# Kernel optimization log

Hardware: AMD Instinct MI355X
Metric: run time of the kernel (lower is better)

The kernel has to match this reference:

```python
import jax, jax.numpy as jnp
import numpy as np

N_NODES = 20000
N_EDGES = 640000
IN_DIM = 128
HID = 128
OUT_DIM = 3
N_GRAPHS = 32


def setup_inputs() -> dict:
    key = jax.random.key(0)
    ks = jax.random.split(key, 12)
    x = jax.random.normal(ks[0], (N_NODES, IN_DIM), dtype=jnp.float32)
    edge_index = jax.random.randint(ks[1], (2, N_EDGES), 0, N_NODES, dtype=jnp.int64)
    batch = jnp.sort(jax.random.randint(ks[2], (N_NODES,), 0, N_GRAPHS, dtype=jnp.int64))
    batch = batch.at[0].set(0).at[-1].set(N_GRAPHS - 1)
    s = 0.05
    W_gcn = jax.random.normal(ks[3], (IN_DIM, HID), jnp.float32) * s
    b_gcn = jnp.zeros((HID,), jnp.float32)
    W_sage_l = jax.random.normal(ks[4], (HID, HID), jnp.float32) * s  # neighbor branch
    W_sage_r = jax.random.normal(ks[5], (HID, HID), jnp.float32) * s  # root branch
    b_sage = jnp.zeros((HID,), jnp.float32)
    W_fc1 = jax.random.normal(ks[6], (HID, HID), jnp.float32) * s
    b_fc1 = jnp.zeros((HID,), jnp.float32)
    W_fc2 = jax.random.normal(ks[7], (HID, OUT_DIM), jnp.float32) * s
    b_fc2 = jnp.zeros((OUT_DIM,), jnp.float32)
    return {
        'x': x, 'edge_index': edge_index, 'batch': batch,
        'W_gcn': W_gcn, 'b_gcn': b_gcn,
        'W_sage_l': W_sage_l, 'W_sage_r': W_sage_r, 'b_sage': b_sage,
        'W_fc1': W_fc1, 'b_fc1': b_fc1, 'W_fc2': W_fc2, 'b_fc2': b_fc2,
    }


def reference(x, edge_index, batch, W_gcn, b_gcn, W_sage_l, W_sage_r, b_sage,
              W_fc1, b_fc1, W_fc2, b_fc2):
    n = x.shape[0]
    row, col = edge_index[0], edge_index[1]  # source -> target

    # ---- GCNConv: symmetric-normalized aggregation with self-loops ----
    h = x @ W_gcn  # [N, H]
    loops = jnp.arange(n, dtype=row.dtype)
    row_sl = jnp.concatenate([row, loops])
    col_sl = jnp.concatenate([col, loops])
    deg = jax.ops.segment_sum(jnp.ones_like(col_sl, dtype=h.dtype), col_sl,
                              num_segments=n)
    dinv = jnp.where(deg > 0, jax.lax.rsqrt(deg), 0.0)
    norm = dinv[row_sl] * dinv[col_sl]  # [E+N]
    h_gcn = jax.ops.segment_sum(h[row_sl] * norm[:, None], col_sl,
                                num_segments=n) + b_gcn
    h_gcn = jax.nn.relu(h_gcn)

    # ---- SAGEConv (mean aggregator) ----
    cnt = jax.ops.segment_sum(jnp.ones_like(col, dtype=h_gcn.dtype), col,
                              num_segments=n)
    neigh = jax.ops.segment_sum(h_gcn[row], col, num_segments=n)
    neigh = neigh / jnp.maximum(cnt, 1.0)[:, None]
    h_sage = neigh @ W_sage_l + h_gcn @ W_sage_r + b_sage
    h_sage = jax.nn.relu(h_sage)

    # ---- global_add_pool (num_graphs = 32 < 50) ----
    pooled = jax.ops.segment_sum(h_sage, batch, num_segments=N_GRAPHS)  # [G, H]

    # ---- MLP head ----
    out = jax.nn.relu(pooled @ W_fc1 + b_fc1) @ W_fc2 + b_fc2  # [G, 3]
    return out
```

## Files before the change

### kernel.cpp

```cpp
#include <hip/hip_runtime.h>

#define N_NODES 20000
#define N_EDGES 640000
#define HID 128
#define N_GRAPHS 32

#define SCAN_BLK 256
#define SCAN_NBLK ((N_NODES + SCAN_BLK - 1) / SCAN_BLK)

__global__ __launch_bounds__(256) void hist_k(const int* __restrict__ col,
                                              int* __restrict__ cnt) {
    int e = blockIdx.x * blockDim.x + threadIdx.x;
    if (e < N_EDGES) {
        int c = col[e];
        if ((unsigned)c < N_NODES) atomicAdd(&cnt[c], 1);
    }
}

__global__ __launch_bounds__(SCAN_BLK) void scanA_k(const int* __restrict__ cnt,
                                                    int* __restrict__ blkSum) {
    __shared__ int wsum[SCAN_BLK / 64];
    const int b = blockIdx.x, t = threadIdx.x;
    const int i = b * SCAN_BLK + t;
    int v = (i < N_NODES) ? cnt[i] : 0;
#pragma unroll
    for (int o = 1; o < 64; o <<= 1) v += __shfl_xor(v, o);
    if ((t & 63) == 0) wsum[t >> 6] = v;
    __syncthreads();
    if (t == 0) {
        int s = 0;
#pragma unroll
        for (int w = 0; w < SCAN_BLK / 64; ++w) s += wsum[w];
        blkSum[b] = s;
    }
}

__global__ __launch_bounds__(SCAN_BLK) void scanB_k(const int* __restrict__ cnt,
                                                    const int* __restrict__ blkSum,
                                                    int* __restrict__ offs,
                                                    int* __restrict__ cursor,
                                                    float* __restrict__ dinv) {
    __shared__ int sm[SCAN_BLK];
    __shared__ int base_s;
    const int b = blockIdx.x, t = threadIdx.x;
    const int i = b * SCAN_BLK + t;
    const int v = (i < N_NODES) ? cnt[i] : 0;
    sm[t] = v;
    if (t == 0) {
        int s = 0;
        for (int k = 0; k < b; ++k) s += blkSum[k];
        base_s = s;
    }
    __syncthreads();
    for (int o = 1; o < SCAN_BLK; o <<= 1) {
        int add = (t >= o) ? sm[t - o] : 0;
        __syncthreads();
        sm[t] += add;
        __syncthreads();
    }
    if (i < N_NODES) {
        int excl = base_s + ((t > 0) ? sm[t - 1] : 0);
        offs[i] = excl;
        cursor[i] = excl;
        dinv[i] = rsqrtf((float)(v + 1));
        if (i == N_NODES - 1) offs[N_NODES] = excl + v;
    }
}

__global__ __launch_bounds__(256) void fill_k(const int* __restrict__ row,
                                              const int* __restrict__ col,
                                              int* __restrict__ cursor,
                                              int* __restrict__ csr_src) {
    int e = blockIdx.x * blockDim.x + threadIdx.x;
    if (e < N_EDGES) {
        int c = col[e];
        int r = row[e];
        if ((unsigned)c < N_NODES && (unsigned)r < N_NODES) {
            int p = atomicAdd(&cursor[c], 1);
            csr_src[p] = r;
        }
    }
}

__global__ __launch_bounds__(256) void gemm128_k(const float* __restrict__ X,
                                                 const float* __restrict__ W,
                                                 float* __restrict__ Y,
                                                 int nrows) {
    __shared__ float ws[128 * 128];
    __shared__ float xs[32 * 128];
    const int t = threadIdx.x;
    for (int i = t; i < 4096; i += 256)
        ((float4*)ws)[i] = ((const float4*)W)[i];
    const int rg = t >> 5;
    const int c4 = (t & 31) * 4;
    const int ntiles = (nrows + 31) / 32;
    for (int tile = blockIdx.x; tile < ntiles; tile += gridDim.x) {
        const int row0 = tile * 32;
        __syncthreads();
#pragma unroll
        for (int i = 0; i < 4; ++i) {
            int idx = t + i * 256;
            int rr = row0 + (idx >> 5);
            float4 v = (rr < nrows) ? ((const float4*)X)[(size_t)rr * 32 + (idx & 31)]
                                    : make_float4(0.f, 0.f, 0.f, 0.f);
            ((float4*)xs)[idx] = v;
        }
        __syncthreads();
        float4 acc[4];
        acc[0] = acc[1] = acc[2] = acc[3] = make_float4(0.f, 0.f, 0.f, 0.f);
#pragma unroll 4
        for (int k = 0; k < 128; k += 2) {
            float4 w0 = *(const float4*)&ws[(k + 0) * 128 + c4];
            float4 w1 = *(const float4*)&ws[(k + 1) * 128 + c4];
#pragma unroll
            for (int i = 0; i < 4; ++i) {
                float2 xv = *(const float2*)&xs[(rg * 4 + i) * 128 + k];
                acc[i].x = fmaf(xv.x, w0.x, fmaf(xv.y, w1.x, acc[i].x));
                acc[i].y = fmaf(xv.x, w0.y, fmaf(xv.y, w1.y, acc[i].y));
                acc[i].z = fmaf(xv.x, w0.z, fmaf(xv.y, w1.z, acc[i].z));
                acc[i].w = fmaf(xv.x, w0.w, fmaf(xv.y, w1.w, acc[i].w));
            }
        }
#pragma unroll
        for (int i = 0; i < 4; ++i) {
            int rr = row0 + rg * 4 + i;
            if (rr < nrows) *(float4*)&Y[(size_t)rr * 128 + c4] = acc[i];
        }
    }
}

__global__ __launch_bounds__(256) void gcn_agg_k(const float* __restrict__ h,
                                                 const int* __restrict__ offs,
                                                 const int* __restrict__ src,
                                                 const float* __restrict__ dinv,
                                                 const float* __restrict__ bias,
                                                 float* __restrict__ out) {
    const int wave = threadIdx.x >> 6;
    const int lane = threadIdx.x & 63;
    const int half = lane >> 5;
    const int node = (blockIdx.x * 4 + wave) * 2 + half;
    const int c4 = (lane & 31) * 4;
    const int nd = (node < N_NODES) ? node : (N_NODES - 1);
    const float dc = dinv[nd];
    float4 hv = *(const float4*)&h[(size_t)nd * 128 + c4];
    float4 acc = make_float4(dc * hv.x, dc * hv.y, dc * hv.z, dc * hv.w);
    const int beg = offs[nd];
    const int deg = offs[nd + 1] - beg;
    const int mdeg = max(deg, __shfl(deg, lane ^ 32));
    for (int j = 0; j < mdeg; j += 4) {
        int i0 = (j + 0 < deg) ? beg + j + 0 : 0;
        int i1 = (j + 1 < deg) ? beg + j + 1 : 0;
        int i2 = (j + 2 < deg) ? beg + j + 2 : 0;
        int i3 = (j + 3 < deg) ? beg + j + 3 : 0;
        int s0 = src[i0], s1 = src[i1], s2 = src[i2], s3 = src[i3];
        float w0 = (j + 0 < deg) ? dinv[s0] : 0.f;
        float w1 = (j + 1 < deg) ? dinv[s1] : 0.f;
        float w2 = (j + 2 < deg) ? dinv[s2] : 0.f;
        float w3 = (j + 3 < deg) ? dinv[s3] : 0.f;
        float4 v0 = *(const float4*)&h[(size_t)s0 * 128 + c4];
        float4 v1 = *(const float4*)&h[(size_t)s1 * 128 + c4];
        float4 v2 = *(const float4*)&h[(size_t)s2 * 128 + c4];
        float4 v3 = *(const float4*)&h[(size_t)s3 * 128 + c4];
        acc.x = fmaf(w0, v0.x, fmaf(w1, v1.x, fmaf(w2, v2.x, fmaf(w3, v3.x, acc.x))));
        acc.y = fmaf(w0, v0.y, fmaf(w1, v1.y, fmaf(w2, v2.y, fmaf(w3, v3.y, acc.y))));
        acc.z = fmaf(w0, v0.z, fmaf(w1, v1.z, fmaf(w2, v2.z, fmaf(w3, v3.z, acc.z))));
        acc.w = fmaf(w0, v0.w, fmaf(w1, v1.w, fmaf(w2, v2.w, fmaf(w3, v3.w, acc.w))));
    }
    float4 b = *(const float4*)&bias[c4];
    float4 o;
    o.x = fmaxf(fmaf(dc, acc.x, b.x), 0.f);
    o.y = fmaxf(fmaf(dc, acc.y, b.y), 0.f);
    o.z = fmaxf(fmaf(dc, acc.z, b.z), 0.f);
    o.w = fmaxf(fmaf(dc, acc.w, b.w), 0.f);
    if (node < N_NODES) *(float4*)&out[(size_t)node * 128 + c4] = o;
}

__global__ __launch_bounds__(256) void sage_agg_k(const float* __restrict__ hg,
                                                  const int* __restrict__ offs,
                                                  const int* __restrict__ src,
                                                  float* __restrict__ out) {
    const int wave = threadIdx.x >> 6;
    const int lane = threadIdx.x & 63;
    const int half = lane >> 5;
    const int node = (blockIdx.x * 4 + wave) * 2 + half;
    const int c4 = (lane & 31) * 4;
    const int nd = (node < N_NODES) ? node : (N_NODES - 1);
    float4 acc = make_float4(0.f, 0.f, 0.f, 0.f);
    const int beg = offs[nd];
    const int deg = offs[nd + 1] - beg;
    const int mdeg = max(deg, __shfl(deg, lane ^ 32));
    for (int j = 0; j < mdeg; j += 4) {
        int i0 = (j + 0 < deg) ? beg + j + 0 : 0;
        int i1 = (j + 1 < deg) ? beg + j + 1 : 0;
        int i2 = (j + 2 < deg) ? beg + j + 2 : 0;
        int i3 = (j + 3 < deg) ? beg + j + 3 : 0;
        float w0 = (j + 0 < deg) ? 1.f : 0.f;
        float w1 = (j + 1 < deg) ? 1.f : 0.f;
        float w2 = (j + 2 < deg) ? 1.f : 0.f;
        float w3 = (j + 3 < deg) ? 1.f : 0.f;
        int s0 = src[i0], s1 = src[i1], s2 = src[i2], s3 = src[i3];
        float4 v0 = *(const float4*)&hg[(size_t)s0 * 128 + c4];
        float4 v1 = *(const float4*)&hg[(size_t)s1 * 128 + c4];
        float4 v2 = *(const float4*)&hg[(size_t)s2 * 128 + c4];
        float4 v3 = *(const float4*)&hg[(size_t)s3 * 128 + c4];
        acc.x = fmaf(w0, v0.x, fmaf(w1, v1.x, fmaf(w2, v2.x, fmaf(w3, v3.x, acc.x))));
        acc.y = fmaf(w0, v0.y, fmaf(w1, v1.y, fmaf(w2, v2.y, fmaf(w3, v3.y, acc.y))));
        acc.z = fmaf(w0, v0.z, fmaf(w1, v1.z, fmaf(w2, v2.z, fmaf(w3, v3.z, acc.z))));
        acc.w = fmaf(w0, v0.w, fmaf(w1, v1.w, fmaf(w2, v2.w, fmaf(w3, v3.w, acc.w))));
    }
    float inv = 1.0f / (float)max(deg, 1);
    float4 o;
    o.x = acc.x * inv;
    o.y = acc.y * inv;
    o.z = acc.z * inv;
    o.w = acc.w * inv;
    if (node < N_NODES) *(float4*)&out[(size_t)node * 128 + c4] = o;
}

__global__ __launch_bounds__(256) void combine_k(const float* __restrict__ An,
                                                 const float* __restrict__ Bh,
                                                 const float* __restrict__ Wl,
                                                 const float* __restrict__ Wr,
                                                 const float* __restrict__ bias,
                                                 float* __restrict__ Y) {
    __shared__ float ws[128 * 128];
    __shared__ float xs[32 * 128];
    const int t = threadIdx.x;
    const int rg = t >> 5;
    const int c4 = (t & 31) * 4;
    const int ntiles = (N_NODES + 31) / 32;
    for (int tile = blockIdx.x; tile < ntiles; tile += gridDim.x) {
        const int row0 = tile * 32;
        float4 acc[4];
        {
            float4 b = *(const float4*)&bias[c4];
            acc[0] = acc[1] = acc[2] = acc[3] = b;
        }
#pragma unroll
        for (int m = 0; m < 2; ++m) {
            const float* Wm = m ? Wr : Wl;
            const float* Xm = m ? Bh : An;
            __syncthreads();
            for (int i = t; i < 4096; i += 256)
                ((float4*)ws)[i] = ((const float4*)Wm)[i];
#pragma unroll
            for (int i = 0; i < 4; ++i) {
                int idx = t + i * 256;
                int rr = row0 + (idx >> 5);
                float4 v = (rr < N_NODES) ? ((const float4*)Xm)[(size_t)rr * 32 + (idx & 31)]
                                          : make_float4(0.f, 0.f, 0.f, 0.f);
                ((float4*)xs)[idx] = v;
            }
            __syncthreads();
#pragma unroll 4
            for (int k = 0; k < 128; k += 2) {
                float4 w0 = *(const float4*)&ws[(k + 0) * 128 + c4];
                float4 w1 = *(const float4*)&ws[(k + 1) * 128 + c4];
#pragma unroll
                for (int i = 0; i < 4; ++i) {
                    float2 xv = *(const float2*)&xs[(rg * 4 + i) * 128 + k];
                    acc[i].x = fmaf(xv.x, w0.x, fmaf(xv.y, w1.x, acc[i].x));
                    acc[i].y = fmaf(xv.x, w0.y, fmaf(xv.y, w1.y, acc[i].y));
                    acc[i].z = fmaf(xv.x, w0.z, fmaf(xv.y, w1.z, acc[i].z));
                    acc[i].w = fmaf(xv.x, w0.w, fmaf(xv.y, w1.w, acc[i].w));
                }
            }
        }
#pragma unroll
        for (int i = 0; i < 4; ++i) {
            int rr = row0 + rg * 4 + i;
            if (rr < N_NODES) {
                float4 o = acc[i];
                o.x = fmaxf(o.x, 0.f);
                o.y = fmaxf(o.y, 0.f);
                o.z = fmaxf(o.z, 0.f);
                o.w = fmaxf(o.w, 0.f);
                *(float4*)&Y[(size_t)rr * 128 + c4] = o;
            }
        }
    }
}

#define POOL_ROWS 64
__global__ __launch_bounds__(256) void pool_k(const float* __restrict__ H,
                                              const int* __restrict__ batch,
                                              float* __restrict__ pooled) {
    const int r0 = blockIdx.x * POOL_ROWS;
    const int t = threadIdx.x;
    const int d = t & 127, half = t >> 7;
    const int rend = min(r0 + POOL_ROWS, N_NODES);
    int i = r0 + half;
    if (i >= rend) return;
    int cur = batch[i];
    float acc = 0.f;
    for (; i < rend; i += 2) {
        int g = batch[i];
        if (g != cur) {
            atomicAdd(&pooled[cur * 128 + d], acc);
            acc = 0.f;
            cur = g;
        }
        acc += H[(size_t)i * 128 + d];
    }
    atomicAdd(&pooled[cur * 128 + d], acc);
}

__global__ __launch_bounds__(128) void head_k(const float* __restrict__ pooled,
                                              const float* __restrict__ Wfc1,
                                              const float* __restrict__ bfc1,
                                              const float* __restrict__ Wfc2,
                                              const float* __restrict__ bfc2,
                                              float* __restrict__ out) {
    __shared__ float pl[128];
    __shared__ float tmp[128];
    const int g = blockIdx.x;
    const int t = threadIdx.x;
    pl[t] = pooled[g * 128 + t];
    __syncthreads();
    float a = bfc1[t];
#pragma unroll 8
    for (int k = 0; k < 128; ++k) a = fmaf(pl[k], Wfc1[k * 128 + t], a);
    tmp[t] = fmaxf(a, 0.f);
    __syncthreads();
    if (t < 3) {
        float a2 = bfc2[t];
        for (int k = 0; k < 128; ++k) a2 = fmaf(tmp[k], Wfc2[k * 3 + t], a2);
        out[g * 3 + t] = a2;
    }
}

extern "C" void kernel_launch(void* const* d_in, const int* in_sizes, int n_in,
                              void* d_out, int out_size, void* d_ws, size_t ws_size,
                              hipStream_t stream) {
    const float* x      = (const float*)d_in[0];
    const int*   ei     = (const int*)d_in[1];
    const int*   batch  = (const int*)d_in[2];
    const float* W_gcn  = (const float*)d_in[3];
    const float* b_gcn  = (const float*)d_in[4];
    const float* W_sl   = (const float*)d_in[5];
    const float* W_sr   = (const float*)d_in[6];
    const float* b_sage = (const float*)d_in[7];
    const float* W_fc1  = (const float*)d_in[8];
    const float* b_fc1  = (const float*)d_in[9];
    const float* W_fc2  = (const float*)d_in[10];
    const float* b_fc2  = (const float*)d_in[11];
    float* out = (float*)d_out;

    char* base = (char*)d_ws;
    size_t off = 0;
    auto take = [&](size_t bytes) -> void* {
        void* p = base + off;
        off += (bytes + 255) & ~(size_t)255;
        return p;
    };
    int*   cnt      = (int*)take((size_t)N_NODES * 4);
    int*   offs     = (int*)take((size_t)(N_NODES + 1) * 4);
    int*   cursor   = (int*)take((size_t)N_NODES * 4);
    float* dinv     = (float*)take((size_t)N_NODES * 4);
    int*   blkSum   = (int*)take((size_t)SCAN_NBLK * 4);
    int*   csr_src  = (int*)take((size_t)N_EDGES * 4);
    float* bufA     = (float*)take((size_t)N_NODES * HID * 4);
    float* bufB     = (float*)take((size_t)N_NODES * HID * 4);
    float* pooled   = (float*)take((size_t)N_GRAPHS * HID * 4);

    const int* row = ei;
    const int* col = ei + N_EDGES;

    hipMemsetAsync(cnt, 0, (size_t)N_NODES * 4, stream);
    hipMemsetAsync(pooled, 0, (size_t)N_GRAPHS * HID * 4, stream);

    hist_k<<<(N_EDGES + 255) / 256, 256, 0, stream>>>(col, cnt);
    scanA_k<<<SCAN_NBLK, SCAN_BLK, 0, stream>>>(cnt, blkSum);
    scanB_k<<<SCAN_NBLK, SCAN_BLK, 0, stream>>>(cnt, blkSum, offs, cursor, dinv);
    fill_k<<<(N_EDGES + 255) / 256, 256, 0, stream>>>(row, col, cursor, csr_src);

    const int ntiles = (N_NODES + 31) / 32;
    const int agg_blocks = (N_NODES + 7) / 8;
    gemm128_k<<<ntiles, 256, 0, stream>>>(x, W_gcn, bufA, N_NODES);
    gcn_agg_k<<<agg_blocks, 256, 0, stream>>>(bufA, offs, csr_src, dinv, b_gcn, bufB);
    sage_agg_k<<<agg_blocks, 256, 0, stream>>>(bufB, offs, csr_src, bufA);
    combine_k<<<ntiles, 256, 0, stream>>>(bufA, bufB, W_sl, W_sr, b_sage, bufA);
    pool_k<<<(N_NODES + POOL_ROWS - 1) / POOL_ROWS, 256, 0, stream>>>(bufA, batch, pooled);
    head_k<<<N_GRAPHS, 128, 0, stream>>>(pooled, W_fc1, b_fc1, W_fc2, b_fc2, out);
}
```

Baseline: 316.6 us.

## Restructure node GEMMs to read X directly per wave and stage W in halves

Both the GCN projection GEMM and the SAGE combine GEMM are rewritten. X rows are no longer staged in shared memory: each wave owns 8 rows and reads them as float4 broadcast loads. Each lane computes two output columns, and W is staged in 64-row halves, which halves shared memory per block and should raise occupancy. Bounds checks are dropped because N_NODES divides by 32, and the loads of the same X address across a wave rely on the cache.

```diff
diff --git a/kernel.cpp b/kernel.cpp
--- a/kernel.cpp
+++ b/kernel.cpp
@@ -84,49 +84,45 @@
 
 __global__ __launch_bounds__(256) void gemm128_k(const float* __restrict__ X,
                                                  const float* __restrict__ W,
-                                                 float* __restrict__ Y,
-                                                 int nrows) {
-    __shared__ float ws[128 * 128];
-    __shared__ float xs[32 * 128];
+                                                 float* __restrict__ Y) {
+    __shared__ float wbuf[64 * 128];
     const int t = threadIdx.x;
-    for (int i = t; i < 4096; i += 256)
-        ((float4*)ws)[i] = ((const float4*)W)[i];
-    const int rg = t >> 5;
-    const int c4 = (t & 31) * 4;
-    const int ntiles = (nrows + 31) / 32;
-    for (int tile = blockIdx.x; tile < ntiles; tile += gridDim.x) {
-        const int row0 = tile * 32;
+    const int lane = t & 63;
+    const int wid = __builtin_amdgcn_readfirstlane(t >> 6);
+    const int c2 = lane * 2;
+    const int row0 = blockIdx.x * 32 + wid * 8;
+    const float* Xr = X + (size_t)row0 * 128;
+    float2 acc[8];
+#pragma unroll
+    for (int r = 0; r < 8; ++r) acc[r] = make_float2(0.f, 0.f);
+#pragma unroll
+    for (int kc = 0; kc < 2; ++kc) {
         __syncthreads();
 #pragma unroll
-        for (int i = 0; i < 4; ++i) {
-            int idx = t + i * 256;
-            int rr = row0 + (idx >> 5);
-            float4 v = (rr < nrows) ? ((const float4*)X)[(size_t)rr * 32 + (idx & 31)]
-                                    : make_float4(0.f, 0.f, 0.f, 0.f);
-            ((float4*)xs)[idx] = v;
-        }
+        for (int i = 0; i < 8; ++i)
+            ((float4*)wbuf)[t + i * 256] = ((const float4*)W)[kc * 2048 + t + i * 256];
         __syncthreads();
-        float4 acc[4];
-        acc[0] = acc[1] = acc[2] = acc[3] = make_float4(0.f, 0.f, 0.f, 0.f);
-#pragma unroll 4
-        for (int k = 0; k < 128; k += 2) {
-            float4 w0 = *(const float4*)&ws[(k + 0) * 128 + c4];
-            float4 w1 = *(const float4*)&ws[(k + 1) * 128 + c4];
-#pragma unroll
-            for (int i = 0; i < 4; ++i) {
-                float2 xv = *(const float2*)&xs[(rg * 4 + i) * 128 + k];
-                acc[i].x = fmaf(xv.x, w0.x, fmaf(xv.y, w1.x, acc[i].x));
-                acc[i].y = fmaf(xv.x, w0.y, fmaf(xv.y, w1.y, acc[i].y));
-                acc[i].z = fmaf(xv.x, w0.z, fmaf(xv.y, w1.z, acc[i].z));
-                acc[i].w = fmaf(xv.x, w0.w, fmaf(xv.y, w1.w, acc[i].w));
+        const int kb = kc * 64;
+        for (int k0 = 0; k0 < 64; k0 += 4) {
+            float4 xa[8];
+#pragma unroll
+            for (int r = 0; r < 8; ++r)
+                xa[r] = *(const float4*)&Xr[r * 128 + kb + k0];
+#pragma unroll
+            for (int kk = 0; kk < 4; ++kk) {
+                float2 w = *(const float2*)&wbuf[(k0 + kk) * 128 + c2];
+#pragma unroll
+                for (int r = 0; r < 8; ++r) {
+                    float xv = (&xa[r].x)[kk];
+                    acc[r].x = fmaf(xv, w.x, acc[r].x);
+                    acc[r].y = fmaf(xv, w.y, acc[r].y);
+                }
             }
         }
-#pragma unroll
-        for (int i = 0; i < 4; ++i) {
-            int rr = row0 + rg * 4 + i;
-            if (rr < nrows) *(float4*)&Y[(size_t)rr * 128 + c4] = acc[i];
-        }
-    }
+    }
+#pragma unroll
+    for (int r = 0; r < 8; ++r)
+        *(float2*)&Y[(size_t)(row0 + r) * 128 + c2] = acc[r];
 }
 
 __global__ __launch_bounds__(256) void gcn_agg_k(const float* __restrict__ h,
@@ -223,61 +219,54 @@
                                                  const float* __restrict__ Wr,
                                                  const float* __restrict__ bias,
                                                  float* __restrict__ Y) {
-    __shared__ float ws[128 * 128];
-    __shared__ float xs[32 * 128];
+    __shared__ float wbuf[64 * 128];
     const int t = threadIdx.x;
-    const int rg = t >> 5;
-    const int c4 = (t & 31) * 4;
-    const int ntiles = (N_NODES + 31) / 32;
-    for (int tile = blockIdx.x; tile < ntiles; tile += gridDim.x) {
-        const int row0 = tile * 32;
-        float4 acc[4];
-        {
-            float4 b = *(const float4*)&bias[c4];
-            acc[0] = acc[1] = acc[2] = acc[3] = b;
-        }
-#pragma unroll
-        for (int m = 0; m < 2; ++m) {
-            const float* Wm = m ? Wr : Wl;
-            const float* Xm = m ? Bh : An;
+    const int lane = t & 63;
+    const int wid = __builtin_amdgcn_readfirstlane(t >> 6);
+    const int c2 = lane * 2;
+    const int row0 = blockIdx.x * 32 + wid * 8;
+    float2 acc[8];
+    {
+        float2 b = *(const float2*)&bias[c2];
+#pragma unroll
+        for (int r = 0; r < 8; ++r) acc[r] = b;
+    }
+#pragma unroll
+    for (int m = 0; m < 2; ++m) {
+        const float* Wm = m ? Wr : Wl;
+        const float* Xr = (m ? Bh : An) + (size_t)row0 * 128;
+#pragma unroll
+        for (int kc = 0; kc < 2; ++kc) {
             __syncthreads();
-            for (int i = t; i < 4096; i += 256)
-                ((float4*)ws)[i] = ((const float4*)Wm)[i];
-#pragma unroll
-            for (int i = 0; i < 4; ++i) {
-                int idx = t + i * 256;
-                int rr = row0 + (idx >> 5);
-                float4 v = (rr < N_NODES) ? ((const float4*)Xm)[(size_t)rr * 32 + (idx & 31)]
-                                          : make_float4(0.f, 0.f, 0.f, 0.f);
-                ((float4*)xs)[idx] = v;
-            }
+#pragma unroll
+            for (int i = 0; i < 8; ++i)
+                ((float4*)wbuf)[t + i * 256] = ((const float4*)Wm)[kc * 2048 + t + i * 256];
             __syncthreads();
-#pragma unroll 4
-            for (int k = 0; k < 128; k += 2) {
-                float4 w0 = *(const float4*)&ws[(k + 0) * 128 + c4];
-                float4 w1 = *(const float4*)&ws[(k + 1) * 128 + c4];
-#pragma unroll
-                for (int i = 0; i < 4; ++i) {
-                    float2 xv = *(const float2*)&xs[(rg * 4 + i) * 128 + k];
-                    acc[i].x = fmaf(xv.x, w0.x, fmaf(xv.y, w1.x, acc[i].x));
-                    acc[i].y = fmaf(xv.x, w0.y, fmaf(xv.y, w1.y, acc[i].y));
-                    acc[i].z = fmaf(xv.x, w0.z, fmaf(xv.y, w1.z, acc[i].z));
-                    acc[i].w = fmaf(xv.x, w0.w, fmaf(xv.y, w1.w, acc[i].w));
+            const int kb = kc * 64;
+            for (int k0 = 0; k0 < 64; k0 += 4) {
+                float4 xa[8];
+#pragma unroll
+                for (int r = 0; r < 8; ++r)
+                    xa[r] = *(const float4*)&Xr[r * 128 + kb + k0];
+#pragma unroll
+                for (int kk = 0; kk < 4; ++kk) {
+                    float2 w = *(const float2*)&wbuf[(k0 + kk) * 128 + c2];
+#pragma unroll
+                    for (int r = 0; r < 8; ++r) {
+                        float xv = (&xa[r].x)[kk];
+                        acc[r].x = fmaf(xv, w.x, acc[r].x);
+                        acc[r].y = fmaf(xv, w.y, acc[r].y);
+                    }
                 }
             }
         }
-#pragma unroll
-        for (int i = 0; i < 4; ++i) {
-            int rr = row0 + rg * 4 + i;
-            if (rr < N_NODES) {
-                float4 o = acc[i];
-                o.x = fmaxf(o.x, 0.f);
-                o.y = fmaxf(o.y, 0.f);
-                o.z = fmaxf(o.z, 0.f);
-                o.w = fmaxf(o.w, 0.f);
-                *(float4*)&Y[(size_t)rr * 128 + c4] = o;
-            }
-        }
+    }
+#pragma unroll
+    for (int r = 0; r < 8; ++r) {
+        float2 o = acc[r];
+        o.x = fmaxf(o.x, 0.f);
+        o.y = fmaxf(o.y, 0.f);
+        *(float2*)&Y[(size_t)(row0 + r) * 128 + c2] = o;
     }
 }
 
@@ -374,12 +363,12 @@
     scanB_k<<<SCAN_NBLK, SCAN_BLK, 0, stream>>>(cnt, blkSum, offs, cursor, dinv);
     fill_k<<<(N_EDGES + 255) / 256, 256, 0, stream>>>(row, col, cursor, csr_src);
 
-    const int ntiles = (N_NODES + 31) / 32;
+    const int gemm_blocks = N_NODES / 32;
     const int agg_blocks = (N_NODES + 7) / 8;
-    gemm128_k<<<ntiles, 256, 0, stream>>>(x, W_gcn, bufA, N_NODES);
+    gemm128_k<<<gemm_blocks, 256, 0, stream>>>(x, W_gcn, bufA);
     gcn_agg_k<<<agg_blocks, 256, 0, stream>>>(bufA, offs, csr_src, dinv, b_gcn, bufB);
     sage_agg_k<<<agg_blocks, 256, 0, stream>>>(bufB, offs, csr_src, bufA);
-    combine_k<<<ntiles, 256, 0, stream>>>(bufA, bufB, W_sl, W_sr, b_sage, bufA);
+    combine_k<<<gemm_blocks, 256, 0, stream>>>(bufA, bufB, W_sl, W_sr, b_sage, bufA);
     pool_k<<<(N_NODES + POOL_ROWS - 1) / POOL_ROWS, 256, 0, stream>>>(bufA, batch, pooled);
     head_k<<<N_GRAPHS, 128, 0, stream>>>(pooled, W_fc1, b_fc1, W_fc2, b_fc2, out);
 }
```

Result: slower. 330.0 us (+4.2%).
